# Kernel optimization log

Measured on AMD Instinct MI355X. Metric: run time of the kernel, lower is better.

Reference implementation:

```python
import jax, jax.numpy as jnp
import numpy as np

B, S, E, H = 4, 2048, 1024, 16
D = E // H  # head_size = 64


def setup_inputs() -> dict:
    key = jax.random.key(0)
    ks = jax.random.split(key, 8)
    s = 1.0 / np.sqrt(E)
    return {
        "values": jax.random.normal(ks[0], (B, S, E), jnp.float32),
        "keys": jax.random.normal(ks[1], (B, S, E), jnp.float32),
        "queries": jax.random.normal(ks[2], (B, S, E), jnp.float32),
        "Wv": jax.random.normal(ks[3], (E, E), jnp.float32) * s,
        "Wk": jax.random.normal(ks[4], (E, E), jnp.float32) * s,
        "Wq": jax.random.normal(ks[5], (E, E), jnp.float32) * s,
        "Wo": jax.random.normal(ks[6], (E, E), jnp.float32) * s,
        "bo": jax.random.normal(ks[7], (E,), jnp.float32) * s,
    }


def reference(values, keys, queries, Wv, Wk, Wq, Wo, bo):
    # torch Linear: y = x @ W.T
    k = (keys @ Wk.T).reshape(B, S, H, D).transpose(0, 2, 1, 3)    # [B,H,S,D]
    q = (queries @ Wq.T).reshape(B, S, H, D).transpose(0, 2, 1, 3)
    v = (values @ Wv.T).reshape(B, S, H, D).transpose(0, 2, 1, 3)
    dot = jnp.einsum('bhqd,bhkd->bhqk', q, k)                      # raw logits
    # NOTE: softmax BEFORE scaling (faithful to original module)
    probs = jax.nn.softmax(dot, axis=-1) / jnp.sqrt(jnp.float32(D))
    out = jnp.einsum('bhqk,bhkd->bhqd', probs, v)                  # [B,H,S,D]
    out = out.transpose(0, 2, 1, 3).reshape(B, S, E)
    return out @ Wo.T + bo
```

## Files before the change

kernel.cpp:

```cpp
#include <hip/hip_runtime.h>
#include <stdint.h>

#define NB 4
#define NS 2048
#define NE 1024
#define NH 16
#define ND 64

typedef __attribute__((ext_vector_type(8))) short short8;
typedef __attribute__((ext_vector_type(2))) float f32x2;
typedef __attribute__((ext_vector_type(4))) float f32x4;
typedef __attribute__((ext_vector_type(8))) float f32x8;
typedef __attribute__((ext_vector_type(16))) float f32x16;
typedef __attribute__((ext_vector_type(4))) unsigned short us4;
typedef __attribute__((ext_vector_type(4))) unsigned int u32x4;
typedef __attribute__((ext_vector_type(2))) __bf16 bf16x2;

#define LOG2E 1.4426950408889634f

__device__ __forceinline__ unsigned short f2bf(float f) {
    return __builtin_bit_cast(unsigned short, static_cast<__bf16>(f));
}
__device__ __forceinline__ unsigned int packbf(float lo, float hi_) {
    f32x2 v; v[0] = lo; v[1] = hi_;
    return __builtin_bit_cast(unsigned int, __builtin_convertvector(v, bf16x2));
}
__device__ __forceinline__ float exp2n(float x) {
    float y;
    asm("v_exp_f32 %0, %1" : "=v"(y) : "v"(x));
    return y;
}

__global__ __launch_bounds__(256) void cvt_w4_kernel(const float* __restrict__ w0,
                                                     const float* __restrict__ w1,
                                                     const float* __restrict__ w2,
                                                     const float* __restrict__ w3,
                                                     unsigned short* __restrict__ d0,
                                                     unsigned short* __restrict__ d1,
                                                     unsigned short* __restrict__ d2,
                                                     unsigned short* __restrict__ d3) {
    const int g = blockIdx.x >> 10;
    const float* src = g == 0 ? w0 : g == 1 ? w1 : g == 2 ? w2 : w3;
    unsigned short* dst = g == 0 ? d0 : g == 1 ? d1 : g == 2 ? d2 : d3;
    const float scl = (g == 2) ? LOG2E : 1.0f;
    const int i = ((blockIdx.x & 1023) * 256 + threadIdx.x) * 4;
    f32x4 f = *(const f32x4*)(src + i);
    us4 o;
#pragma unroll
    for (int j = 0; j < 4; ++j) o[j] = f2bf(f[j] * scl);
    *(us4*)(dst + i) = o;
}

template<int A_IS_F32, int OUT_MODE>
__global__ __launch_bounds__(256) void gemm_bt(const void* __restrict__ Aptr,
                                               const unsigned short* __restrict__ Wp,
                                               void* __restrict__ Cp,
                                               const float* __restrict__ bias) {
    constexpr int K = 1024;
    __shared__ unsigned short As[128][40];
    __shared__ unsigned short Bs[128][40];
    const int tid = threadIdx.x;
    const int bm = blockIdx.x, bn = blockIdx.y;
    const int lane = tid & 63, wid = tid >> 6;
    const int lr = lane & 15, lg = lane >> 4;
    const int wr = wid >> 1, wc = wid & 1;
    const int srow = tid >> 1, shalf = tid & 1;

    f32x4 acc[4][4];
#pragma unroll
    for (int a = 0; a < 4; ++a)
#pragma unroll
        for (int b = 0; b < 4; ++b) acc[a][b] = (f32x4){0.f, 0.f, 0.f, 0.f};

    const size_t arow = (size_t)(bm * 128 + srow) * K + shalf * 16;
    const size_t brow = (size_t)(bn * 128 + srow) * K + shalf * 16;
    const float*          apF = (const float*)Aptr + arow;
    const unsigned short* apH = (const unsigned short*)Aptr + arow;
    const unsigned short* bp  = Wp + brow;

    f32x4 pa0, pa1, pa2, pa3;
    short8 pah0, pah1, pb0, pb1;
    if (A_IS_F32) {
        pa0 = *(const f32x4*)(apF);
        pa1 = *(const f32x4*)(apF + 4);
        pa2 = *(const f32x4*)(apF + 8);
        pa3 = *(const f32x4*)(apF + 12);
    } else {
        pah0 = *(const short8*)(apH);
        pah1 = *(const short8*)(apH + 8);
    }
    pb0 = *(const short8*)(bp);
    pb1 = *(const short8*)(bp + 8);

    for (int k0 = 0; k0 < K; k0 += 32) {
        __syncthreads();
        if (A_IS_F32) {
            short8 p0, p1;
#pragma unroll
            for (int j = 0; j < 4; ++j) {
                p0[j]     = (short)f2bf(pa0[j]);
                p0[j + 4] = (short)f2bf(pa1[j]);
                p1[j]     = (short)f2bf(pa2[j]);
                p1[j + 4] = (short)f2bf(pa3[j]);
            }
            *(short8*)&As[srow][shalf * 16]     = p0;
            *(short8*)&As[srow][shalf * 16 + 8] = p1;
        } else {
            *(short8*)&As[srow][shalf * 16]     = pah0;
            *(short8*)&As[srow][shalf * 16 + 8] = pah1;
        }
        *(short8*)&Bs[srow][shalf * 16]     = pb0;
        *(short8*)&Bs[srow][shalf * 16 + 8] = pb1;
        __syncthreads();

        if (k0 + 32 < K) {
            const int kn = k0 + 32;
            if (A_IS_F32) {
                pa0 = *(const f32x4*)(apF + kn);
                pa1 = *(const f32x4*)(apF + kn + 4);
                pa2 = *(const f32x4*)(apF + kn + 8);
                pa3 = *(const f32x4*)(apF + kn + 12);
            } else {
                pah0 = *(const short8*)(apH + kn);
                pah1 = *(const short8*)(apH + kn + 8);
            }
            pb0 = *(const short8*)(bp + kn);
            pb1 = *(const short8*)(bp + kn + 8);
        }

        short8 af[4], bfr[4];
#pragma unroll
        for (int mi = 0; mi < 4; ++mi) af[mi]  = *(const short8*)&As[wr * 64 + mi * 16 + lr][lg * 8];
#pragma unroll
        for (int ni = 0; ni < 4; ++ni) bfr[ni] = *(const short8*)&Bs[wc * 64 + ni * 16 + lr][lg * 8];
#pragma unroll
        for (int mi = 0; mi < 4; ++mi)
#pragma unroll
            for (int ni = 0; ni < 4; ++ni)
                acc[mi][ni] = __builtin_amdgcn_mfma_f32_16x16x32_bf16(af[mi], bfr[ni], acc[mi][ni], 0, 0, 0);
    }

#pragma unroll
    for (int mi = 0; mi < 4; ++mi) {
#pragma unroll
        for (int ni = 0; ni < 4; ++ni) {
            const int n = bn * 128 + wc * 64 + ni * 16 + lr;
            if (OUT_MODE == 2) {
                const int m0 = bm * 128 + wr * 64 + mi * 16 + lg * 4;
                const int b = m0 >> 11, s0 = m0 & 2047;
                const int h = n >> 6, d = n & 63;
                us4 pk;
#pragma unroll
                for (int i = 0; i < 4; ++i) pk[i] = f2bf(acc[mi][ni][i]);
                const size_t idx = ((((size_t)b * NH + h) * (NS / 64) + (s0 >> 6)) * ND + d) * 64 + (s0 & 63);
                *(us4*)&((unsigned short*)Cp)[idx] = pk;
            } else {
#pragma unroll
                for (int i = 0; i < 4; ++i) {
                    const int m = bm * 128 + wr * 64 + mi * 16 + lg * 4 + i;
                    const float val = acc[mi][ni][i];
                    if (OUT_MODE == 0) {
                        const int b = m >> 11, s = m & 2047, h = n >> 6, d = n & 63;
                        ((unsigned short*)Cp)[(((size_t)b * NH + h) * NS + s) * ND + d] = f2bf(val);
                    } else {
                        ((float*)Cp)[(size_t)m * 1024 + n] = val + bias[n];
                    }
                }
            }
        }
    }
}

__global__ __launch_bounds__(256, 4) void attn_kernel(const unsigned short* __restrict__ q,
                                                      const unsigned short* __restrict__ k,
                                                      const unsigned short* __restrict__ vtt,
                                                      unsigned short* __restrict__ o) {
    __shared__ unsigned short Kl[64][72];
    __shared__ unsigned short Vl[64][72];
    const int tid = threadIdx.x;
    const int lane = tid & 63, wid = tid >> 6;
    const int l31 = lane & 31, hi = lane >> 5;
    const int bh = blockIdx.y;
    const int qw = blockIdx.x * 128 + wid * 32;
    const size_t base = (size_t)bh * NS * ND;

    short8 qf[4];
    {
        const unsigned short* qp = q + base + (size_t)(qw + l31) * ND + 8 * hi;
#pragma unroll
        for (int m = 0; m < 4; ++m) qf[m] = *(const short8*)(qp + 16 * m);
    }

    float l_run = 0.f;
    f32x16 oa0, oa1, fz;
#pragma unroll
    for (int i = 0; i < 16; ++i) { oa0[i] = 0.f; oa1[i] = 0.f; fz[i] = 0.f; }

    const int strow = tid >> 2, stcol = (tid & 3) * 16;
    const unsigned short* ks = k   + base + tid * 16;
    const unsigned short* vs = vtt + base + tid * 16;

    short8 kr0 = *(const short8*)(ks);
    short8 kr1 = *(const short8*)(ks + 8);
    short8 vr0 = *(const short8*)(vs);
    short8 vr1 = *(const short8*)(vs + 8);

    for (int kv0 = 0; kv0 < NS; kv0 += 64) {
        __syncthreads();
        *(short8*)&Kl[strow][stcol]     = kr0;
        *(short8*)&Kl[strow][stcol + 8] = kr1;
        *(short8*)&Vl[strow][stcol]     = vr0;
        *(short8*)&Vl[strow][stcol + 8] = vr1;
        __syncthreads();

        if (kv0 + 64 < NS) {
            const unsigned short* ks2 = ks + (size_t)(kv0 + 64) * ND;
            const unsigned short* vs2 = vs + (size_t)(kv0 + 64) * ND;
            kr0 = *(const short8*)(ks2);
            kr1 = *(const short8*)(ks2 + 8);
            vr0 = *(const short8*)(vs2);
            vr1 = *(const short8*)(vs2 + 8);
        }

        f32x16 st0, st1;
        __builtin_amdgcn_s_setprio(1);
        {
            short8 kf;
            kf = *(const short8*)&Kl[l31][8 * hi];
            st0 = __builtin_amdgcn_mfma_f32_32x32x16_bf16(kf, qf[0], fz, 0, 0, 0);
            kf = *(const short8*)&Kl[l31][16 + 8 * hi];
            st0 = __builtin_amdgcn_mfma_f32_32x32x16_bf16(kf, qf[1], st0, 0, 0, 0);
            kf = *(const short8*)&Kl[l31][32 + 8 * hi];
            st0 = __builtin_amdgcn_mfma_f32_32x32x16_bf16(kf, qf[2], st0, 0, 0, 0);
            kf = *(const short8*)&Kl[l31][48 + 8 * hi];
            st0 = __builtin_amdgcn_mfma_f32_32x32x16_bf16(kf, qf[3], st0, 0, 0, 0);
            kf = *(const short8*)&Kl[32 + l31][8 * hi];
            st1 = __builtin_amdgcn_mfma_f32_32x32x16_bf16(kf, qf[0], fz, 0, 0, 0);
            kf = *(const short8*)&Kl[32 + l31][16 + 8 * hi];
            st1 = __builtin_amdgcn_mfma_f32_32x32x16_bf16(kf, qf[1], st1, 0, 0, 0);
            kf = *(const short8*)&Kl[32 + l31][32 + 8 * hi];
            st1 = __builtin_amdgcn_mfma_f32_32x32x16_bf16(kf, qf[2], st1, 0, 0, 0);
            kf = *(const short8*)&Kl[32 + l31][48 + 8 * hi];
            st1 = __builtin_amdgcn_mfma_f32_32x32x16_bf16(kf, qf[3], st1, 0, 0, 0);
        }
        __builtin_amdgcn_s_setprio(0);

        st0 = st0 - 64.0f;
        st1 = st1 - 64.0f;
#pragma unroll
        for (int i = 0; i < 16; ++i) st0[i] = exp2n(st0[i]);
#pragma unroll
        for (int i = 0; i < 16; ++i) st1[i] = exp2n(st1[i]);
        {
            f32x16 sv = st0 + st1;
            f32x8 s8 = __builtin_shufflevector(sv, sv, 0, 1, 2, 3, 4, 5, 6, 7)
                     + __builtin_shufflevector(sv, sv, 8, 9, 10, 11, 12, 13, 14, 15);
            f32x4 s4 = __builtin_shufflevector(s8, s8, 0, 1, 2, 3)
                     + __builtin_shufflevector(s8, s8, 4, 5, 6, 7);
            f32x2 s2 = __builtin_shufflevector(s4, s4, 0, 1)
                     + __builtin_shufflevector(s4, s4, 2, 3);
            float rs = s2[0] + s2[1];
            rs += __shfl_xor(rs, 32, 64);
            l_run += rs;
        }

        short8 pf0, pf1, pf2, pf3;
#define MKPF(PF, SV, RB) { \
        unsigned int wa = packbf(SV[RB + 0], SV[RB + 1]); \
        unsigned int wb = packbf(SV[RB + 2], SV[RB + 3]); \
        unsigned int wc = packbf(SV[RB + 4], SV[RB + 5]); \
        unsigned int wd = packbf(SV[RB + 6], SV[RB + 7]); \
        asm("v_permlane32_swap_b32 %0, %1" : "+v"(wa), "+v"(wc)); \
        asm("v_permlane32_swap_b32 %0, %1" : "+v"(wb), "+v"(wd)); \
        u32x4 pw; pw[0] = wa; pw[1] = wb; pw[2] = wc; pw[3] = wd; \
        PF = __builtin_bit_cast(short8, pw); }
        MKPF(pf0, st0, 0)
        MKPF(pf1, st0, 8)
        MKPF(pf2, st1, 0)
        MKPF(pf3, st1, 8)
#undef MKPF

        __builtin_amdgcn_s_setprio(1);
        {
            short8 vf;
            vf = *(const short8*)&Vl[l31][8 * hi];
            oa0 = __builtin_amdgcn_mfma_f32_32x32x16_bf16(vf, pf0, oa0, 0, 0, 0);
            vf = *(const short8*)&Vl[l31][16 + 8 * hi];
            oa0 = __builtin_amdgcn_mfma_f32_32x32x16_bf16(vf, pf1, oa0, 0, 0, 0);
            vf = *(const short8*)&Vl[l31][32 + 8 * hi];
            oa0 = __builtin_amdgcn_mfma_f32_32x32x16_bf16(vf, pf2, oa0, 0, 0, 0);
            vf = *(const short8*)&Vl[l31][48 + 8 * hi];
            oa0 = __builtin_amdgcn_mfma_f32_32x32x16_bf16(vf, pf3, oa0, 0, 0, 0);
            vf = *(const short8*)&Vl[32 + l31][8 * hi];
            oa1 = __builtin_amdgcn_mfma_f32_32x32x16_bf16(vf, pf0, oa1, 0, 0, 0);
            vf = *(const short8*)&Vl[32 + l31][16 + 8 * hi];
            oa1 = __builtin_amdgcn_mfma_f32_32x32x16_bf16(vf, pf1, oa1, 0, 0, 0);
            vf = *(const short8*)&Vl[32 + l31][32 + 8 * hi];
            oa1 = __builtin_amdgcn_mfma_f32_32x32x16_bf16(vf, pf2, oa1, 0, 0, 0);
            vf = *(const short8*)&Vl[32 + l31][48 + 8 * hi];
            oa1 = __builtin_amdgcn_mfma_f32_32x32x16_bf16(vf, pf3, oa1, 0, 0, 0);
        }
        __builtin_amdgcn_s_setprio(0);
    }

    const int b = bh >> 4, h = bh & 15;
    const float scl = 0.125f / l_run;
    unsigned short* op = o + (((size_t)b * NS + (qw + l31)) * NH + h) * ND;
#pragma unroll
    for (int rq = 0; rq < 4; ++rq) {
        us4 p0, p1;
#pragma unroll
        for (int i = 0; i < 4; ++i) {
            p0[i] = f2bf(oa0[4 * rq + i] * scl);
            p1[i] = f2bf(oa1[4 * rq + i] * scl);
        }
        *(us4*)&op[8 * rq + 4 * hi]      = p0;
        *(us4*)&op[32 + 8 * rq + 4 * hi] = p1;
    }
}

extern "C" void kernel_launch(void* const* d_in, const int* in_sizes, int n_in,
                              void* d_out, int out_size, void* d_ws, size_t ws_size,
                              hipStream_t stream) {
    (void)in_sizes; (void)n_in; (void)out_size; (void)ws_size;
    const float* values  = (const float*)d_in[0];
    const float* keys    = (const float*)d_in[1];
    const float* queries = (const float*)d_in[2];
    const float* Wv = (const float*)d_in[3];
    const float* Wk = (const float*)d_in[4];
    const float* Wq = (const float*)d_in[5];
    const float* Wo = (const float*)d_in[6];
    const float* bo = (const float*)d_in[7];

    uint8_t* ws = (uint8_t*)d_ws;
    const size_t MB = (size_t)1 << 20;
    unsigned short* wvb = (unsigned short*)(ws + 0 * MB);
    unsigned short* wkb = (unsigned short*)(ws + 2 * MB);
    unsigned short* wqb = (unsigned short*)(ws + 4 * MB);
    unsigned short* wob = (unsigned short*)(ws + 6 * MB);
    unsigned short* qb  = (unsigned short*)(ws + 8 * MB);
    unsigned short* kb  = (unsigned short*)(ws + 24 * MB);
    unsigned short* vtb = (unsigned short*)(ws + 40 * MB);
    unsigned short* ab  = (unsigned short*)(ws + 56 * MB);

    cvt_w4_kernel<<<4096, 256, 0, stream>>>(Wv, Wk, Wq, Wo, wvb, wkb, wqb, wob);

    dim3 gg(64, 8);
    gemm_bt<1, 0><<<gg, 256, 0, stream>>>(queries, wqb, qb,  nullptr);
    gemm_bt<1, 0><<<gg, 256, 0, stream>>>(keys,    wkb, kb,  nullptr);
    gemm_bt<1, 2><<<gg, 256, 0, stream>>>(values,  wvb, vtb, nullptr);

    attn_kernel<<<dim3(16, 64), 256, 0, stream>>>(qb, kb, vtb, ab);

    gemm_bt<0, 1><<<gg, 256, 0, stream>>>(ab, wob, d_out, bo);
}
```

Baseline: 229.7 us.

## Pre-convert activations to bf16 and use direct global-to-LDS double-buffered GEMM

After: 218.9 us. -4.7%, faster.

```diff
diff --git a/kernel.cpp b/kernel.cpp
--- a/kernel.cpp
+++ b/kernel.cpp
@@ -30,41 +30,68 @@
     asm("v_exp_f32 %0, %1" : "=v"(y) : "v"(x));
     return y;
 }
-
-__global__ __launch_bounds__(256) void cvt_w4_kernel(const float* __restrict__ w0,
-                                                     const float* __restrict__ w1,
-                                                     const float* __restrict__ w2,
-                                                     const float* __restrict__ w3,
-                                                     unsigned short* __restrict__ d0,
-                                                     unsigned short* __restrict__ d1,
-                                                     unsigned short* __restrict__ d2,
-                                                     unsigned short* __restrict__ d3) {
-    const int g = blockIdx.x >> 10;
-    const float* src = g == 0 ? w0 : g == 1 ? w1 : g == 2 ? w2 : w3;
-    unsigned short* dst = g == 0 ? d0 : g == 1 ? d1 : g == 2 ? d2 : d3;
-    const float scl = (g == 2) ? LOG2E : 1.0f;
-    const int i = ((blockIdx.x & 1023) * 256 + threadIdx.x) * 4;
-    f32x4 f = *(const f32x4*)(src + i);
+__device__ __forceinline__ void gl_lds16(const void* g, void* l) {
+    __builtin_amdgcn_global_load_lds(
+        (const __attribute__((address_space(1))) unsigned int*)g,
+        (__attribute__((address_space(3))) unsigned int*)l, 16, 0, 0);
+}
+
+__global__ __launch_bounds__(256) void cvt_all_kernel(
+    const float* __restrict__ w0, const float* __restrict__ w1,
+    const float* __restrict__ w2, const float* __restrict__ w3,
+    const float* __restrict__ x0, const float* __restrict__ x1,
+    const float* __restrict__ x2,
+    unsigned short* __restrict__ dw0, unsigned short* __restrict__ dw1,
+    unsigned short* __restrict__ dw2, unsigned short* __restrict__ dw3,
+    unsigned short* __restrict__ dx0, unsigned short* __restrict__ dx1,
+    unsigned short* __restrict__ dx2) {
+    const int bid = blockIdx.x;
+    const float* src;
+    unsigned short* dst;
+    int idx;
+    float scl = 1.0f;
+    if (bid < 4096) {
+        const int g = bid >> 10;
+        src = g == 0 ? w0 : g == 1 ? w1 : g == 2 ? w2 : w3;
+        dst = g == 0 ? dw0 : g == 1 ? dw1 : g == 2 ? dw2 : dw3;
+        if (g == 2) scl = LOG2E;
+        idx = ((bid & 1023) * 256 + threadIdx.x) * 4;
+    } else {
+        const int b2 = bid - 4096;
+        const int g = b2 >> 13;
+        src = g == 0 ? x0 : g == 1 ? x1 : x2;
+        dst = g == 0 ? dx0 : g == 1 ? dx1 : dx2;
+        idx = ((b2 & 8191) * 256 + threadIdx.x) * 4;
+    }
+    f32x4 f = *(const f32x4*)(src + idx);
     us4 o;
 #pragma unroll
     for (int j = 0; j < 4; ++j) o[j] = f2bf(f[j] * scl);
-    *(us4*)(dst + i) = o;
-}
-
-template<int A_IS_F32, int OUT_MODE>
-__global__ __launch_bounds__(256) void gemm_bt(const void* __restrict__ Aptr,
-                                               const unsigned short* __restrict__ Wp,
-                                               void* __restrict__ Cp,
-                                               const float* __restrict__ bias) {
-    constexpr int K = 1024;
-    __shared__ unsigned short As[128][40];
-    __shared__ unsigned short Bs[128][40];
+    *(us4*)(dst + idx) = o;
+}
+
+struct GemmArgs {
+    const unsigned short *a0, *a1, *a2;
+    const unsigned short *w0, *w1, *w2;
+    void *c0, *c1, *c2;
+    const float* bias;
+};
+
+template<int OUT_SEL>
+__global__ __launch_bounds__(256) void gemm_glds(GemmArgs args) {
+    __shared__ __align__(16) unsigned short As[2][4096];
+    __shared__ __align__(16) unsigned short Bs[2][4096];
     const int tid = threadIdx.x;
-    const int bm = blockIdx.x, bn = blockIdx.y;
+    const int bm = blockIdx.x, bn = blockIdx.y, z = blockIdx.z;
+    const unsigned short* Ab = z == 0 ? args.a0 : z == 1 ? args.a1 : args.a2;
+    const unsigned short* Wb = z == 0 ? args.w0 : z == 1 ? args.w1 : args.w2;
+    void* Cp               = z == 0 ? args.c0 : z == 1 ? args.c1 : args.c2;
     const int lane = tid & 63, wid = tid >> 6;
     const int lr = lane & 15, lg = lane >> 4;
     const int wr = wid >> 1, wc = wid & 1;
-    const int srow = tid >> 1, shalf = tid & 1;
+
+    const size_t aoff = (size_t)(bm * 128 + (tid >> 2)) * 1024 + (tid & 3) * 8;
+    const size_t boff = (size_t)(bn * 128 + (tid >> 2)) * 1024 + (tid & 3) * 8;
 
     f32x4 acc[4][4];
 #pragma unroll
@@ -72,80 +99,46 @@
 #pragma unroll
         for (int b = 0; b < 4; ++b) acc[a][b] = (f32x4){0.f, 0.f, 0.f, 0.f};
 
-    const size_t arow = (size_t)(bm * 128 + srow) * K + shalf * 16;
-    const size_t brow = (size_t)(bn * 128 + srow) * K + shalf * 16;
-    const float*          apF = (const float*)Aptr + arow;
-    const unsigned short* apH = (const unsigned short*)Aptr + arow;
-    const unsigned short* bp  = Wp + brow;
-
-    f32x4 pa0, pa1, pa2, pa3;
-    short8 pah0, pah1, pb0, pb1;
-    if (A_IS_F32) {
-        pa0 = *(const f32x4*)(apF);
-        pa1 = *(const f32x4*)(apF + 4);
-        pa2 = *(const f32x4*)(apF + 8);
-        pa3 = *(const f32x4*)(apF + 12);
-    } else {
-        pah0 = *(const short8*)(apH);
-        pah1 = *(const short8*)(apH + 8);
-    }
-    pb0 = *(const short8*)(bp);
-    pb1 = *(const short8*)(bp + 8);
-
-    for (int k0 = 0; k0 < K; k0 += 32) {
-        __syncthreads();
-        if (A_IS_F32) {
-            short8 p0, p1;
-#pragma unroll
-            for (int j = 0; j < 4; ++j) {
-                p0[j]     = (short)f2bf(pa0[j]);
-                p0[j + 4] = (short)f2bf(pa1[j]);
-                p1[j]     = (short)f2bf(pa2[j]);
-                p1[j + 4] = (short)f2bf(pa3[j]);
-            }
-            *(short8*)&As[srow][shalf * 16]     = p0;
-            *(short8*)&As[srow][shalf * 16 + 8] = p1;
-        } else {
-            *(short8*)&As[srow][shalf * 16]     = pah0;
-            *(short8*)&As[srow][shalf * 16 + 8] = pah1;
-        }
-        *(short8*)&Bs[srow][shalf * 16]     = pb0;
-        *(short8*)&Bs[srow][shalf * 16 + 8] = pb1;
-        __syncthreads();
-
-        if (k0 + 32 < K) {
-            const int kn = k0 + 32;
-            if (A_IS_F32) {
-                pa0 = *(const f32x4*)(apF + kn);
-                pa1 = *(const f32x4*)(apF + kn + 4);
-                pa2 = *(const f32x4*)(apF + kn + 8);
-                pa3 = *(const f32x4*)(apF + kn + 12);
-            } else {
-                pah0 = *(const short8*)(apH + kn);
-                pah1 = *(const short8*)(apH + kn + 8);
-            }
-            pb0 = *(const short8*)(bp + kn);
-            pb1 = *(const short8*)(bp + kn + 8);
-        }
-
+#define STAGE(buf, kk) { \
+    gl_lds16(Ab + aoff + (kk),             &As[buf][tid * 8]); \
+    gl_lds16(Ab + aoff + 64 * 1024 + (kk), &As[buf][2048 + tid * 8]); \
+    gl_lds16(Wb + boff + (kk),             &Bs[buf][tid * 8]); \
+    gl_lds16(Wb + boff + 64 * 1024 + (kk), &Bs[buf][2048 + tid * 8]); }
+
+    STAGE(0, 0)
+    __syncthreads();
+    int cur = 0;
+    for (int k0 = 0; k0 < 1024; k0 += 32) {
+        if (k0 + 32 < 1024) STAGE(cur ^ 1, k0 + 32)
         short8 af[4], bfr[4];
 #pragma unroll
-        for (int mi = 0; mi < 4; ++mi) af[mi]  = *(const short8*)&As[wr * 64 + mi * 16 + lr][lg * 8];
-#pragma unroll
-        for (int ni = 0; ni < 4; ++ni) bfr[ni] = *(const short8*)&Bs[wc * 64 + ni * 16 + lr][lg * 8];
+        for (int mi = 0; mi < 4; ++mi)
+            af[mi] = *(const short8*)&As[cur][(wr * 64 + mi * 16 + lr) * 32 + lg * 8];
+#pragma unroll
+        for (int ni = 0; ni < 4; ++ni)
+            bfr[ni] = *(const short8*)&Bs[cur][(wc * 64 + ni * 16 + lr) * 32 + lg * 8];
 #pragma unroll
         for (int mi = 0; mi < 4; ++mi)
 #pragma unroll
             for (int ni = 0; ni < 4; ++ni)
                 acc[mi][ni] = __builtin_amdgcn_mfma_f32_16x16x32_bf16(af[mi], bfr[ni], acc[mi][ni], 0, 0, 0);
-    }
+        __syncthreads();
+        cur ^= 1;
+    }
+#undef STAGE
 
 #pragma unroll
     for (int mi = 0; mi < 4; ++mi) {
 #pragma unroll
         for (int ni = 0; ni < 4; ++ni) {
             const int n = bn * 128 + wc * 64 + ni * 16 + lr;
-            if (OUT_MODE == 2) {
+            if (OUT_SEL == 1) {
+#pragma unroll
+                for (int i = 0; i < 4; ++i) {
+                    const int m = bm * 128 + wr * 64 + mi * 16 + lg * 4 + i;
+                    ((float*)Cp)[(size_t)m * 1024 + n] = acc[mi][ni][i] + args.bias[n];
+                }
+            } else if (z == 2) {
                 const int m0 = bm * 128 + wr * 64 + mi * 16 + lg * 4;
                 const int b = m0 >> 11, s0 = m0 & 2047;
                 const int h = n >> 6, d = n & 63;
@@ -158,13 +151,8 @@
 #pragma unroll
                 for (int i = 0; i < 4; ++i) {
                     const int m = bm * 128 + wr * 64 + mi * 16 + lg * 4 + i;
-                    const float val = acc[mi][ni][i];
-                    if (OUT_MODE == 0) {
-                        const int b = m >> 11, s = m & 2047, h = n >> 6, d = n & 63;
-                        ((unsigned short*)Cp)[(((size_t)b * NH + h) * NS + s) * ND + d] = f2bf(val);
-                    } else {
-                        ((float*)Cp)[(size_t)m * 1024 + n] = val + bias[n];
-                    }
+                    const int b = m >> 11, s = m & 2047, h = n >> 6, d = n & 63;
+                    ((unsigned short*)Cp)[(((size_t)b * NH + h) * NS + s) * ND + d] = f2bf(acc[mi][ni][i]);
                 }
             }
         }
@@ -343,14 +331,26 @@
     unsigned short* vtb = (unsigned short*)(ws + 40 * MB);
     unsigned short* ab  = (unsigned short*)(ws + 56 * MB);
 
-    cvt_w4_kernel<<<4096, 256, 0, stream>>>(Wv, Wk, Wq, Wo, wvb, wkb, wqb, wob);
-
-    dim3 gg(64, 8);
-    gemm_bt<1, 0><<<gg, 256, 0, stream>>>(queries, wqb, qb,  nullptr);
-    gemm_bt<1, 0><<<gg, 256, 0, stream>>>(keys,    wkb, kb,  nullptr);
-    gemm_bt<1, 2><<<gg, 256, 0, stream>>>(values,  wvb, vtb, nullptr);
+    unsigned short* aq = (unsigned short*)d_out;
+    unsigned short* ak = (unsigned short*)d_out + 8388608;
+    unsigned short* av = ab;
+
+    cvt_all_kernel<<<28672, 256, 0, stream>>>(Wv, Wk, Wq, Wo, queries, keys, values,
+                                              wvb, wkb, wqb, wob, aq, ak, av);
+
+    GemmArgs gqkv;
+    gqkv.a0 = aq;  gqkv.a1 = ak;  gqkv.a2 = av;
+    gqkv.w0 = wqb; gqkv.w1 = wkb; gqkv.w2 = wvb;
+    gqkv.c0 = qb;  gqkv.c1 = kb;  gqkv.c2 = vtb;
+    gqkv.bias = nullptr;
+    gemm_glds<0><<<dim3(64, 8, 3), 256, 0, stream>>>(gqkv);
 
     attn_kernel<<<dim3(16, 64), 256, 0, stream>>>(qb, kb, vtb, ab);
 
-    gemm_bt<0, 1><<<gg, 256, 0, stream>>>(ab, wob, d_out, bo);
-}
+    GemmArgs ge;
+    ge.a0 = ge.a1 = ge.a2 = ab;
+    ge.w0 = ge.w1 = ge.w2 = wob;
+    ge.c0 = ge.c1 = ge.c2 = d_out;
+    ge.bias = bo;
+    gemm_glds<1><<<dim3(64, 8, 1), 256, 0, stream>>>(ge);
+}
```
